# Optimization experiments

Measured on AMD Instinct MI355X. Metric: run time of the kernel, lower is better.

Reference implementation:

```python
import jax, jax.numpy as jnp
import numpy as np

DIM = 768
N_HEADS = 12
HEAD_DIM = DIM // N_HEADS

def setup_inputs() -> dict:
    key = jax.random.key(0)
    ks = jax.random.split(key, 5)
    B, N = 8, 1024
    s = 0.02
    x = jax.random.normal(ks[0], (B, N, DIM), dtype=jnp.float32)
    W_qkv = jax.random.normal(ks[1], (DIM, 3 * DIM), dtype=jnp.float32) * s
    b_qkv = jnp.zeros((3 * DIM,), dtype=jnp.float32)
    W_proj = jax.random.normal(ks[2], (DIM, DIM), dtype=jnp.float32) * s
    b_proj = jnp.zeros((DIM,), dtype=jnp.float32)
    return {"x": x, "W_qkv": W_qkv, "b_qkv": b_qkv, "W_proj": W_proj, "b_proj": b_proj}

def reference(x, W_qkv, b_qkv, W_proj, b_proj):
    B, N, D = x.shape
    qkv = x @ W_qkv + b_qkv                                   # [B,N,3D]
    qkv = qkv.reshape(B, N, 3, N_HEADS, HEAD_DIM)
    q, k, v = qkv[:, :, 0], qkv[:, :, 1], qkv[:, :, 2]        # [B,N,H,hd]
    q = q.transpose(0, 2, 1, 3)                               # [B,H,N,hd]
    k = k.transpose(0, 2, 1, 3)
    v = v.transpose(0, 2, 1, 3)
    scores = jnp.einsum('bhqd,bhkd->bhqk', q, k) / jnp.sqrt(jnp.float32(HEAD_DIM))
    attn = jax.nn.softmax(scores, axis=-1)
    out = jnp.einsum('bhqk,bhkd->bhqd', attn, v)              # [B,H,N,hd]
    out = out.transpose(0, 2, 1, 3).reshape(B, N, D)
    return out @ W_proj + b_proj
```

## Files before the change

kernel.cpp:

```cpp
#include <hip/hip_runtime.h>
#include <hip/hip_bf16.h>


typedef __bf16 bf16x8 __attribute__((ext_vector_type(8)));
typedef float f32x4 __attribute__((ext_vector_type(4)));

#define MFMA16(a, b, c) __builtin_amdgcn_mfma_f32_16x16x32_bf16(a, b, c, 0, 0, 0)

#if defined(__has_builtin) && __has_builtin(__builtin_amdgcn_exp2f)
#define EXP2(x) __builtin_amdgcn_exp2f(x)
#else
#define EXP2(x) exp2f(x)
#endif

__device__ inline __bf16 to_bf16(float f) {
  __hip_bfloat16 h = __float2bfloat16(f);
  return *reinterpret_cast<__bf16*>(&h);
}

__device__ __forceinline__ void gload16(const void* g, void* l) {
  __builtin_amdgcn_global_load_lds(
      (const __attribute__((address_space(1))) unsigned int*)(unsigned long long)g,
      (__attribute__((address_space(3))) unsigned int*)(unsigned long long)l,
      16, 0, 0);
}

__global__ void ws_diag_kernel(float* out, int n, float val) {
  int i = blockIdx.x * 256 + threadIdx.x;
  if (i < n) out[i] = val;
}

__global__ __launch_bounds__(256) void prep_kernel(
    const float* __restrict__ x, __hip_bfloat16* __restrict__ xc,
    const float* __restrict__ Wqkv, __hip_bfloat16* __restrict__ WqkvT,
    const float* __restrict__ Wproj, __hip_bfloat16* __restrict__ WprojT) {
  __shared__ __hip_bfloat16 tile[32][33];
  const int b = blockIdx.x;
  if (b < 3072) {
    int i = b * 256 + threadIdx.x;
    float4 a = ((const float4*)x)[i * 2], c = ((const float4*)x)[i * 2 + 1];
    __hip_bfloat16 o[8] = {__float2bfloat16(a.x), __float2bfloat16(a.y),
                           __float2bfloat16(a.z), __float2bfloat16(a.w),
                           __float2bfloat16(c.x), __float2bfloat16(c.y),
                           __float2bfloat16(c.z), __float2bfloat16(c.w)};
    *(int4*)(xc + (size_t)i * 8) = *(const int4*)o;
    return;
  }
  const float* W;
  __hip_bfloat16* Wt;
  int rows, cols, bx, by;
  if (b < 4800) {
    int idx = b - 3072;
    W = Wqkv; Wt = WqkvT; rows = 768; cols = 2304;
    bx = idx % 72; by = idx / 72;
  } else {
    int idx = b - 4800;
    W = Wproj; Wt = WprojT; rows = 768; cols = 768;
    bx = idx % 24; by = idx / 24;
  }
  const int tc = bx * 32, tr = by * 32;
  const int tx = threadIdx.x & 31, ty = threadIdx.x >> 5;
#pragma unroll
  for (int i = 0; i < 4; ++i) {
    int r = ty + i * 8;
    tile[r][tx] = __float2bfloat16(W[(size_t)(tr + r) * cols + tc + tx]);
  }
  __syncthreads();
#pragma unroll
  for (int i = 0; i < 4; ++i) {
    int r = ty + i * 8;
    Wt[(size_t)(tc + r) * rows + tr + tx] = tile[tx][r];
  }
}

__global__ __launch_bounds__(256) void vtrans_kernel(
    const __hip_bfloat16* __restrict__ Vrow, __hip_bfloat16* __restrict__ Vt) {
  constexpr int LP = 72;
  __shared__ __bf16 tile[64 * LP];
  const int tid = threadIdx.x;
  const int bh = blockIdx.x;
  const int n0 = blockIdx.y * 64;
  const size_t base = (size_t)bh << 16;
#pragma unroll
  for (int i = 0; i < 2; ++i) {
    int s = tid + 256 * i;
    int r = s >> 3, c8 = (s & 7) * 8;
    *(int4*)(&tile[r * LP + c8]) =
        *(const int4*)(Vrow + base + (size_t)(n0 + r) * 64 + c8);
  }
  __syncthreads();
#pragma unroll
  for (int i = 0; i < 2; ++i) {
    int s = tid + 256 * i;
    int d = s >> 3, n8 = (s & 7) * 8;
    __bf16 o[8];
#pragma unroll
    for (int j = 0; j < 8; ++j) o[j] = tile[(n8 + j) * LP + d];
    *(int4*)(Vt + base + ((size_t)d << 10) + n0 + n8) = *(const int4*)o;
  }
}

constexpr int GK = 768;

__global__ __launch_bounds__(256) void gemm_qkv_kernel(
    const __hip_bfloat16* __restrict__ A,
    const __hip_bfloat16* __restrict__ Bt,
    const float* __restrict__ bias,
    __hip_bfloat16* __restrict__ Qw,
    __hip_bfloat16* __restrict__ Kw,
    __hip_bfloat16* __restrict__ Vw) {
  __shared__ __align__(16) __bf16 As[128 * 32];
  __shared__ __align__(16) __bf16 Bs[128 * 32];
  const int tid = threadIdx.x;
  const int lane = tid & 63, wave = tid >> 6;
  const int wr = wave >> 1, wc = wave & 1;
  const int m0 = blockIdx.x * 128, n0 = blockIdx.y * 128;
  const int fr = lane & 15, q4 = lane >> 4;

  const int r4 = lane >> 2, c8 = (lane & 3) * 8;
  const __hip_bfloat16* ga0 = A + (size_t)(m0 + wave * 32 + r4) * GK + c8;
  const __hip_bfloat16* gb0 = Bt + (size_t)(n0 + wave * 32 + r4) * GK + c8;
  __bf16* la0 = &As[wave * 1024];
  __bf16* lb0 = &Bs[wave * 1024];

  f32x4 acc[4][4] = {};

  for (int kt = 0; kt < GK / 32; ++kt) {
    __syncthreads();
    gload16(ga0 + kt * 32, la0);
    gload16(ga0 + kt * 32 + 16 * GK, la0 + 512);
    gload16(gb0 + kt * 32, lb0);
    gload16(gb0 + kt * 32 + 16 * GK, lb0 + 512);
    __syncthreads();
    bf16x8 af[4], bfr[4];
#pragma unroll
    for (int i = 0; i < 4; ++i)
      af[i] = *(const bf16x8*)(&As[(wr * 64 + i * 16 + fr) * 32 + q4 * 8]);
#pragma unroll
    for (int j = 0; j < 4; ++j)
      bfr[j] = *(const bf16x8*)(&Bs[(wc * 64 + j * 16 + fr) * 32 + q4 * 8]);
#pragma unroll
    for (int i = 0; i < 4; ++i)
#pragma unroll
      for (int j = 0; j < 4; ++j)
        acc[i][j] = MFMA16(af[i], bfr[j], acc[i][j]);
  }

#pragma unroll
  for (int j = 0; j < 4; ++j) {
    int col = n0 + wc * 64 + j * 16 + fr;
    int which = col / 768;
    int rem = col - which * 768;
    int h = rem >> 6, d = rem & 63;
    float bv = bias[col];
    __hip_bfloat16* dst = (which == 0) ? Qw : (which == 1) ? Kw : Vw;
    float scale = (which == 0) ? 0.18033688011112042f : 1.0f;
#pragma unroll
    for (int i = 0; i < 4; ++i) {
#pragma unroll
      for (int r = 0; r < 4; ++r) {
        int row = m0 + wr * 64 + i * 16 + q4 * 4 + r;
        int bb = row >> 10, nn = row & 1023;
        float v = (acc[i][j][r] + bv) * scale;
        dst[(((size_t)(bb * 12 + h) * 1024 + nn) << 6) + d] = __float2bfloat16(v);
      }
    }
  }
}

__global__ __launch_bounds__(256) void gemm_proj_kernel(
    const __hip_bfloat16* __restrict__ A,
    const __hip_bfloat16* __restrict__ Bt,
    const float* __restrict__ bias,
    float* __restrict__ out) {
  __shared__ __align__(16) __bf16 As[128 * 32];
  __shared__ __align__(16) __bf16 Bs[128 * 32];
  const int tid = threadIdx.x;
  const int lane = tid & 63, wave = tid >> 6;
  const int wr = wave >> 1, wc = wave & 1;
  const int m0 = blockIdx.x * 128, n0 = blockIdx.y * 128;
  const int fr = lane & 15, q4 = lane >> 4;

  const int r4 = lane >> 2, c8 = (lane & 3) * 8;
  const __hip_bfloat16* ga0 = A + (size_t)(m0 + wave * 32 + r4) * GK + c8;
  const __hip_bfloat16* gb0 = Bt + (size_t)(n0 + wave * 32 + r4) * GK + c8;
  __bf16* la0 = &As[wave * 1024];
  __bf16* lb0 = &Bs[wave * 1024];

  f32x4 acc[4][4] = {};

  for (int kt = 0; kt < GK / 32; ++kt) {
    __syncthreads();
    gload16(ga0 + kt * 32, la0);
    gload16(ga0 + kt * 32 + 16 * GK, la0 + 512);
    gload16(gb0 + kt * 32, lb0);
    gload16(gb0 + kt * 32 + 16 * GK, lb0 + 512);
    __syncthreads();
    bf16x8 af[4], bfr[4];
#pragma unroll
    for (int i = 0; i < 4; ++i)
      af[i] = *(const bf16x8*)(&As[(wr * 64 + i * 16 + fr) * 32 + q4 * 8]);
#pragma unroll
    for (int j = 0; j < 4; ++j)
      bfr[j] = *(const bf16x8*)(&Bs[(wc * 64 + j * 16 + fr) * 32 + q4 * 8]);
#pragma unroll
    for (int i = 0; i < 4; ++i)
#pragma unroll
      for (int j = 0; j < 4; ++j)
        acc[i][j] = MFMA16(af[i], bfr[j], acc[i][j]);
  }

#pragma unroll
  for (int j = 0; j < 4; ++j) {
    int col = n0 + wc * 64 + j * 16 + fr;
    float bv = bias[col];
#pragma unroll
    for (int i = 0; i < 4; ++i) {
#pragma unroll
      for (int r = 0; r < 4; ++r) {
        int row = m0 + wr * 64 + i * 16 + q4 * 4 + r;
        out[(size_t)row * 768 + col] = acc[i][j][r] + bv;
      }
    }
  }
}

__global__ __launch_bounds__(512) void attn_kernel(
    const __hip_bfloat16* __restrict__ Qw,
    const __hip_bfloat16* __restrict__ Kw,
    const __hip_bfloat16* __restrict__ Vt,
    __hip_bfloat16* __restrict__ O) {
  constexpr int LP = 72;
  __shared__ __align__(16) __bf16 smem[18432];
  __bf16* Qs = smem;
  __bf16* K1 = smem;
  __bf16* V1 = smem + 4608;
  __bf16* K0 = smem + 9216;
  __bf16* V0 = smem + 13824;
  const int tid = threadIdx.x;
  const int lane = tid & 63, wave = tid >> 6;
  const int fr = lane & 15, q4 = lane >> 4;
  const int bh = blockIdx.x % 96, qt = blockIdx.x / 96;
  const __hip_bfloat16* Qb = Qw + ((size_t)bh * 1024 + qt * 128) * 64;
  const __hip_bfloat16* Kb = Kw + (size_t)bh * 65536;
  const __hip_bfloat16* Vb = Vt + (size_t)bh * 65536;

  const int krow = tid >> 3;
  const int kchunk = ((tid & 7) ^ (krow & 7)) * 8;
  const __hip_bfloat16* ksrc = Kb + (size_t)krow * 64 + kchunk;
  __bf16* kdst0 = K0 + wave * 512;
  __bf16* kdst1 = K1 + wave * 512;
  const int kc = (tid & 7) * 8;
  const int sc8 = tid & 7;
  const int sbase = ((sc8 >> 2) << 5) | ((sc8 & 1) << 4) | (((sc8 >> 1) & 1) << 2);
  const int kx0 = (q4 ^ (fr & 7)) * 8;
  const int kx1 = kx0 ^ 32;

  gload16(ksrc, kdst0);
  int4 vregA = *(const int4*)(Vb + ((size_t)krow << 10) + kc);

#pragma unroll
  for (int i = 0; i < 2; ++i) {
    int s = tid + 512 * i;
    int row = s >> 3, c = (s & 7) * 8;
    *(int4*)(&Qs[row * LP + c]) = *(const int4*)(Qb + row * 64 + c);
  }
  __syncthreads();
  bf16x8 qf[2];
#pragma unroll
  for (int ks = 0; ks < 2; ++ks)
    qf[ks] = *(const bf16x8*)(&Qs[(wave * 16 + fr) * LP + ks * 32 + q4 * 8]);

  float l_i = 0.f;
  f32x4 accO[4] = {};

  *(int2*)(&V0[krow * LP + sbase]) = make_int2(vregA.x, vregA.y);
  *(int2*)(&V0[krow * LP + sbase + 8]) = make_int2(vregA.z, vregA.w);
  int4 vregB = *(const int4*)(Vb + ((size_t)krow << 10) + 64 + kc);
  __syncthreads();

  auto compute_tile = [&](const __bf16* Kbuf, const __bf16* Vbuf) {
    f32x4 scT[4];
    __builtin_amdgcn_s_setprio(1);
#pragma unroll
    for (int nt = 0; nt < 4; ++nt) {
      bf16x8 kf0 = *(const bf16x8*)(&Kbuf[(nt * 16 + fr) * 64 + kx0]);
      bf16x8 kf1 = *(const bf16x8*)(&Kbuf[(nt * 16 + fr) * 64 + kx1]);
      f32x4 z = {};
      z = MFMA16(kf0, qf[0], z);
      scT[nt] = MFMA16(kf1, qf[1], z);
    }
    __builtin_amdgcn_s_setprio(0);
    float rs = 0.f;
#pragma unroll
    for (int nt = 0; nt < 4; ++nt)
#pragma unroll
      for (int r = 0; r < 4; ++r) {
        float p = EXP2(scT[nt][r]);
        scT[nt][r] = p;
        rs += p;
      }
    l_i += rs;
#pragma unroll
    for (int ks = 0; ks < 2; ++ks) {
      bf16x8 pf;
#pragma unroll
      for (int e = 0; e < 4; ++e) {
        pf[e] = to_bf16(scT[2 * ks][e]);
        pf[4 + e] = to_bf16(scT[2 * ks + 1][e]);
      }
      __builtin_amdgcn_s_setprio(1);
#pragma unroll
      for (int dt = 0; dt < 4; ++dt) {
        bf16x8 vf = *(const bf16x8*)(&Vbuf[(dt * 16 + fr) * LP + ks * 32 + q4 * 8]);
        accO[dt] = MFMA16(pf, vf, accO[dt]);
      }
      __builtin_amdgcn_s_setprio(0);
    }
  };

  for (int kt2 = 0; kt2 < 16; kt2 += 2) {
    gload16(ksrc + (size_t)(kt2 + 1) * 4096, kdst1);
    if (kt2 + 2 < 16)
      vregA = *(const int4*)(Vb + ((size_t)krow << 10) + (kt2 + 2) * 64 + kc);
    compute_tile(K0, V0);
    *(int2*)(&V1[krow * LP + sbase]) = make_int2(vregB.x, vregB.y);
    *(int2*)(&V1[krow * LP + sbase + 8]) = make_int2(vregB.z, vregB.w);
    __syncthreads();
    if (kt2 + 2 < 16) {
      gload16(ksrc + (size_t)(kt2 + 2) * 4096, kdst0);
      if (kt2 + 3 < 16)
        vregB = *(const int4*)(Vb + ((size_t)krow << 10) + (kt2 + 3) * 64 + kc);
      compute_tile(K1, V1);
      *(int2*)(&V0[krow * LP + sbase]) = make_int2(vregA.x, vregA.y);
      *(int2*)(&V0[krow * LP + sbase + 8]) = make_int2(vregA.z, vregA.w);
      __syncthreads();
    } else {
      compute_tile(K1, V1);
    }
  }

  l_i += __shfl_xor(l_i, 16, 64);
  l_i += __shfl_xor(l_i, 32, 64);
  float lrow[4];
#pragma unroll
  for (int r = 0; r < 4; ++r) lrow[r] = __shfl(l_i, q4 * 4 + r, 64);

  const int h = bh % 12, bb = bh / 12;
#pragma unroll
  for (int dt = 0; dt < 4; ++dt)
#pragma unroll
    for (int r = 0; r < 4; ++r) {
      int row = bb * 1024 + qt * 128 + wave * 16 + q4 * 4 + r;
      int col = h * 64 + dt * 16 + fr;
      O[(size_t)row * 768 + col] = __float2bfloat16(accO[dt][r] / lrow[r]);
    }
}

extern "C" void kernel_launch(void* const* d_in, const int* in_sizes, int n_in,
                              void* d_out, int out_size, void* d_ws, size_t ws_size,
                              hipStream_t stream) {
  const float* x     = (const float*)d_in[0];
  const float* Wqkv  = (const float*)d_in[1];
  const float* bqkv  = (const float*)d_in[2];
  const float* Wproj = (const float*)d_in[3];
  const float* bproj = (const float*)d_in[4];
  float* out = (float*)d_out;

  constexpr size_t NEEDED = 55050240;
  if (ws_size < NEEDED) {
    ws_diag_kernel<<<(out_size + 255) / 256, 256, 0, stream>>>(
        out, out_size, (float)(ws_size >> 20));
    return;
  }

  char* ws = (char*)d_ws;
  __hip_bfloat16* WqkvT  = (__hip_bfloat16*)(ws);
  __hip_bfloat16* WprojT = (__hip_bfloat16*)(ws + 3538944);
  __hip_bfloat16* Qw     = (__hip_bfloat16*)(ws + 4718592);
  __hip_bfloat16* Kw     = (__hip_bfloat16*)(ws + 17301504);
  __hip_bfloat16* Vrow   = (__hip_bfloat16*)(ws + 29884416);
  __hip_bfloat16* xc     = (__hip_bfloat16*)(ws + 42467328);
  __hip_bfloat16* Vt     = xc;
  __hip_bfloat16* attnO  = Vrow;

  prep_kernel<<<5376, 256, 0, stream>>>(x, xc, Wqkv, WqkvT, Wproj, WprojT);
  gemm_qkv_kernel<<<dim3(64, 18), 256, 0, stream>>>(xc, WqkvT, bqkv, Qw, Kw, Vrow);
  vtrans_kernel<<<dim3(96, 16), 256, 0, stream>>>(Vrow, Vt);
  attn_kernel<<<dim3(96 * 8), 512, 0, stream>>>(Qw, Kw, Vt, attnO);
  gemm_proj_kernel<<<dim3(64, 6), 256, 0, stream>>>(attnO, WprojT, bproj, out);
}
```

Before: 188.1 us.

## Pre-swizzle V tiles in transpose kernel and load via direct global-to-LDS

The V transpose kernel now writes each 64x64 tile already in the XOR-swizzled, k-permuted layout that the attention kernel wants in LDS. The attention kernel can then bring V in with the same async global_load_lds path used for K, instead of loading into registers and scattering into a padded LDS buffer. This removes VGPR staging, the manual LDS stores and the padding, and simplifies the double-buffer loop into a uniform shape. The cost is a more complex write pattern with 8-byte scattered stores in the transpose kernel and a tight coupling between the two kernels' layouts.

```diff
diff --git a/kernel.cpp b/kernel.cpp
--- a/kernel.cpp
+++ b/kernel.cpp
@@ -74,7 +74,7 @@
 }
 
 __global__ __launch_bounds__(256) void vtrans_kernel(
-    const __hip_bfloat16* __restrict__ Vrow, __hip_bfloat16* __restrict__ Vt) {
+    const __hip_bfloat16* __restrict__ Vrow, __hip_bfloat16* __restrict__ Vsig) {
   constexpr int LP = 72;
   __shared__ __bf16 tile[64 * LP];
   const int tid = threadIdx.x;
@@ -92,11 +92,18 @@
 #pragma unroll
   for (int i = 0; i < 2; ++i) {
     int s = tid + 256 * i;
-    int d = s >> 3, n8 = (s & 7) * 8;
+    int d = s >> 3, c = s & 7;
+    int n8 = c * 8;
     __bf16 o[8];
 #pragma unroll
     for (int j = 0; j < 8; ++j) o[j] = tile[(n8 + j) * LP + d];
-    *(int4*)(Vt + base + ((size_t)d << 10) + n0 + n8) = *(const int4*)o;
+    int sb = ((c >> 2) << 5) | ((c & 1) << 4) | (((c >> 1) & 1) << 2);
+    int x = d & 7;
+    int a0 = (((sb >> 3) ^ x) << 3) | (sb & 7);
+    int a1 = ((((sb >> 3) + 1) ^ x) << 3) | (sb & 7);
+    __hip_bfloat16* vr = Vsig + base + (size_t)blockIdx.y * 4096 + d * 64;
+    *(int2*)(vr + a0) = *(const int2*)&o[0];
+    *(int2*)(vr + a1) = *(const int2*)&o[4];
   }
 }
 
@@ -228,36 +235,36 @@
 __global__ __launch_bounds__(512) void attn_kernel(
     const __hip_bfloat16* __restrict__ Qw,
     const __hip_bfloat16* __restrict__ Kw,
-    const __hip_bfloat16* __restrict__ Vt,
+    const __hip_bfloat16* __restrict__ Vsig,
     __hip_bfloat16* __restrict__ O) {
   constexpr int LP = 72;
-  __shared__ __align__(16) __bf16 smem[18432];
+  __shared__ __align__(16) __bf16 smem[17408];
   __bf16* Qs = smem;
   __bf16* K1 = smem;
-  __bf16* V1 = smem + 4608;
+  __bf16* V1 = smem + 4096;
   __bf16* K0 = smem + 9216;
-  __bf16* V0 = smem + 13824;
+  __bf16* V0 = smem + 13312;
   const int tid = threadIdx.x;
   const int lane = tid & 63, wave = tid >> 6;
   const int fr = lane & 15, q4 = lane >> 4;
   const int bh = blockIdx.x % 96, qt = blockIdx.x / 96;
   const __hip_bfloat16* Qb = Qw + ((size_t)bh * 1024 + qt * 128) * 64;
   const __hip_bfloat16* Kb = Kw + (size_t)bh * 65536;
-  const __hip_bfloat16* Vb = Vt + (size_t)bh * 65536;
+  const __hip_bfloat16* Vb = Vsig + (size_t)bh * 65536;
 
   const int krow = tid >> 3;
   const int kchunk = ((tid & 7) ^ (krow & 7)) * 8;
   const __hip_bfloat16* ksrc = Kb + (size_t)krow * 64 + kchunk;
-  __bf16* kdst0 = K0 + wave * 512;
-  __bf16* kdst1 = K1 + wave * 512;
-  const int kc = (tid & 7) * 8;
-  const int sc8 = tid & 7;
-  const int sbase = ((sc8 >> 2) << 5) | ((sc8 & 1) << 4) | (((sc8 >> 1) & 1) << 2);
-  const int kx0 = (q4 ^ (fr & 7)) * 8;
-  const int kx1 = kx0 ^ 32;
-
-  gload16(ksrc, kdst0);
-  int4 vregA = *(const int4*)(Vb + ((size_t)krow << 10) + kc);
+  const __hip_bfloat16* vsrc = Vb + (size_t)tid * 8;
+  __bf16* kd0 = K0 + wave * 512;
+  __bf16* kd1 = K1 + wave * 512;
+  __bf16* vd0 = V0 + wave * 512;
+  __bf16* vd1 = V1 + wave * 512;
+  const int sx0 = (q4 ^ (fr & 7)) * 8;
+  const int sx1 = sx0 ^ 32;
+
+  gload16(ksrc, kd0);
+  gload16(vsrc, vd0);
 
 #pragma unroll
   for (int i = 0; i < 2; ++i) {
@@ -270,22 +277,18 @@
 #pragma unroll
   for (int ks = 0; ks < 2; ++ks)
     qf[ks] = *(const bf16x8*)(&Qs[(wave * 16 + fr) * LP + ks * 32 + q4 * 8]);
+  __syncthreads();
 
   float l_i = 0.f;
   f32x4 accO[4] = {};
-
-  *(int2*)(&V0[krow * LP + sbase]) = make_int2(vregA.x, vregA.y);
-  *(int2*)(&V0[krow * LP + sbase + 8]) = make_int2(vregA.z, vregA.w);
-  int4 vregB = *(const int4*)(Vb + ((size_t)krow << 10) + 64 + kc);
-  __syncthreads();
 
   auto compute_tile = [&](const __bf16* Kbuf, const __bf16* Vbuf) {
     f32x4 scT[4];
     __builtin_amdgcn_s_setprio(1);
 #pragma unroll
     for (int nt = 0; nt < 4; ++nt) {
-      bf16x8 kf0 = *(const bf16x8*)(&Kbuf[(nt * 16 + fr) * 64 + kx0]);
-      bf16x8 kf1 = *(const bf16x8*)(&Kbuf[(nt * 16 + fr) * 64 + kx1]);
+      bf16x8 kf0 = *(const bf16x8*)(&Kbuf[(nt * 16 + fr) * 64 + sx0]);
+      bf16x8 kf1 = *(const bf16x8*)(&Kbuf[(nt * 16 + fr) * 64 + sx1]);
       f32x4 z = {};
       z = MFMA16(kf0, qf[0], z);
       scT[nt] = MFMA16(kf1, qf[1], z);
@@ -312,7 +315,8 @@
       __builtin_amdgcn_s_setprio(1);
 #pragma unroll
       for (int dt = 0; dt < 4; ++dt) {
-        bf16x8 vf = *(const bf16x8*)(&Vbuf[(dt * 16 + fr) * LP + ks * 32 + q4 * 8]);
+        bf16x8 vf = *(const bf16x8*)(
+            &Vbuf[(dt * 16 + fr) * 64 + (ks ? sx1 : sx0)]);
         accO[dt] = MFMA16(pf, vf, accO[dt]);
       }
       __builtin_amdgcn_s_setprio(0);
@@ -320,24 +324,16 @@
   };
 
   for (int kt2 = 0; kt2 < 16; kt2 += 2) {
-    gload16(ksrc + (size_t)(kt2 + 1) * 4096, kdst1);
-    if (kt2 + 2 < 16)
-      vregA = *(const int4*)(Vb + ((size_t)krow << 10) + (kt2 + 2) * 64 + kc);
+    gload16(ksrc + (size_t)(kt2 + 1) * 4096, kd1);
+    gload16(vsrc + (size_t)(kt2 + 1) * 4096, vd1);
     compute_tile(K0, V0);
-    *(int2*)(&V1[krow * LP + sbase]) = make_int2(vregB.x, vregB.y);
-    *(int2*)(&V1[krow * LP + sbase + 8]) = make_int2(vregB.z, vregB.w);
     __syncthreads();
     if (kt2 + 2 < 16) {
-      gload16(ksrc + (size_t)(kt2 + 2) * 4096, kdst0);
-      if (kt2 + 3 < 16)
-        vregB = *(const int4*)(Vb + ((size_t)krow << 10) + (kt2 + 3) * 64 + kc);
-      compute_tile(K1, V1);
-      *(int2*)(&V0[krow * LP + sbase]) = make_int2(vregA.x, vregA.y);
-      *(int2*)(&V0[krow * LP + sbase + 8]) = make_int2(vregA.z, vregA.w);
-      __syncthreads();
-    } else {
-      compute_tile(K1, V1);
-    }
+      gload16(ksrc + (size_t)(kt2 + 2) * 4096, kd0);
+      gload16(vsrc + (size_t)(kt2 + 2) * 4096, vd0);
+    }
+    compute_tile(K1, V1);
+    __syncthreads();
   }
 
   l_i += __shfl_xor(l_i, 16, 64);
@@ -381,12 +377,12 @@
   __hip_bfloat16* Kw     = (__hip_bfloat16*)(ws + 17301504);
   __hip_bfloat16* Vrow   = (__hip_bfloat16*)(ws + 29884416);
   __hip_bfloat16* xc     = (__hip_bfloat16*)(ws + 42467328);
-  __hip_bfloat16* Vt     = xc;
+  __hip_bfloat16* Vsig   = xc;
   __hip_bfloat16* attnO  = Vrow;
 
   prep_kernel<<<5376, 256, 0, stream>>>(x, xc, Wqkv, WqkvT, Wproj, WprojT);
   gemm_qkv_kernel<<<dim3(64, 18), 256, 0, stream>>>(xc, WqkvT, bqkv, Qw, Kw, Vrow);
-  vtrans_kernel<<<dim3(96, 16), 256, 0, stream>>>(Vrow, Vt);
-  attn_kernel<<<dim3(96 * 8), 512, 0, stream>>>(Qw, Kw, Vt, attnO);
+  vtrans_kernel<<<dim3(96, 16), 256, 0, stream>>>(Vrow, Vsig);
+  attn_kernel<<<dim3(96 * 8), 512, 0, stream>>>(Qw, Kw, Vsig, attnO);
   gemm_proj_kernel<<<dim3(64, 6), 256, 0, stream>>>(attnO, WprojT, bproj, out);
 }
```

Measured after the change: 186.4 us. Within noise of the previous version (-0.9%).
